# Performance work log

Hardware: AMD Instinct MI355X
Metric: run time of the kernel (lower is better)

The kernel has to match this reference:

```python
import jax, jax.numpy as jnp
import numpy as np

N_NODES = 100000
N_EDGES = 1600000
IN_FEAT = 64
HEADS = 4
OUT_FEAT = 16
NEG_SLOPE = 0.2  # DGL GATConv default


def setup_inputs() -> dict:
    key = jax.random.key(0)
    ks = jax.random.split(key, 6)
    node_feat = jax.random.normal(ks[0], (N_NODES, IN_FEAT), dtype=jnp.float32)
    W = jax.random.normal(ks[1], (IN_FEAT, HEADS * OUT_FEAT), dtype=jnp.float32) * 0.1
    attn_l = jax.random.normal(ks[2], (HEADS, OUT_FEAT), dtype=jnp.float32) * 0.1
    attn_r = jax.random.normal(ks[3], (HEADS, OUT_FEAT), dtype=jnp.float32) * 0.1
    bias = jnp.zeros((HEADS * OUT_FEAT,), dtype=jnp.float32)
    src = jax.random.randint(ks[4], (N_EDGES,), 0, N_NODES, dtype=jnp.int32)
    dst = jax.random.randint(ks[5], (N_EDGES,), 0, N_NODES, dtype=jnp.int32)
    return {"node_feat": node_feat, "W": W, "attn_l": attn_l, "attn_r": attn_r,
            "bias": bias, "src": src, "dst": dst}


def reference(node_feat, W, attn_l, attn_r, bias, src, dst):
    N = node_feat.shape[0]
    H, F = attn_l.shape
    # linear projection: [N, H, F]
    feat = (node_feat @ W).reshape(N, H, F)
    # per-node attention logits: [N, H]
    el = jnp.einsum('nhf,hf->nh', feat, attn_l)
    er = jnp.einsum('nhf,hf->nh', feat, attn_r)
    # per-edge raw score (src contributes el, dst contributes er): [E, H]
    e = jax.nn.leaky_relu(el[src] + er[dst], NEG_SLOPE)
    # segment softmax over incoming edges of each dst node
    emax = jax.ops.segment_max(e, dst, num_segments=N)           # [N, H]
    emax = jnp.where(jnp.isfinite(emax), emax, 0.0)              # zero-in-degree safety
    ex = jnp.exp(e - emax[dst])                                  # [E, H]
    denom = jax.ops.segment_sum(ex, dst, num_segments=N)         # [N, H]
    alpha = ex / denom[dst]                                      # [E, H]
    # weighted scatter-aggregate of projected src features
    msg = feat[src] * alpha[:, :, None]                          # [E, H, F]
    out = jax.ops.segment_sum(msg, dst, num_segments=N)          # [N, H, F]
    out = out + bias.reshape(1, H, F)
    return out.reshape(N, H * F)
```

## Files before the change

kernel.cpp:

```cpp
#include <hip/hip_runtime.h>
#include <math.h>

#define N_NODES 100000
#define N_EDGES 1600000
#define NEG_SLOPE 0.2f
#define NPASS 1

__global__ __launch_bounds__(256) void k1_project(
        const float* __restrict__ x, const float* __restrict__ W,
        const float* __restrict__ attn_l, const float* __restrict__ attn_r,
        float* __restrict__ feat, float* __restrict__ el, float* __restrict__ er,
        int* __restrict__ deg, int* __restrict__ gtotal) {
    int t    = threadIdx.x;
    int lane = t & 63;
    int wib  = t >> 6;
    int h    = lane >> 4;
    if (blockIdx.x == 0 && t == 0) *gtotal = 0;

    float w[64];
    #pragma unroll
    for (int k = 0; k < 64; ++k) w[k] = W[k * 64 + lane];

    float al = attn_l[lane];
    float ar = attn_r[lane];
    int wavesTotal = (gridDim.x * blockDim.x) >> 6;

    for (int n = blockIdx.x * 4 + wib; n < N_NODES; n += wavesTotal) {
        int nu = __builtin_amdgcn_readfirstlane(n);
        const float4* xr = (const float4*)(x + (size_t)nu * 64);
        float a0 = 0.f, a1 = 0.f, a2 = 0.f, a3 = 0.f;
        #pragma unroll
        for (int kq = 0; kq < 16; ++kq) {
            float4 xq = xr[kq];
            a0 = fmaf(xq.x, w[4 * kq + 0], a0);
            a1 = fmaf(xq.y, w[4 * kq + 1], a1);
            a2 = fmaf(xq.z, w[4 * kq + 2], a2);
            a3 = fmaf(xq.w, w[4 * kq + 3], a3);
        }
        float acc = (a0 + a1) + (a2 + a3);
        feat[n * 64 + lane] = acc;
        float vl = acc * al, vr = acc * ar;
        #pragma unroll
        for (int off = 8; off >= 1; off >>= 1) {
            vl += __shfl_xor(vl, off, 64);
            vr += __shfl_xor(vr, off, 64);
        }
        if ((lane & 15) == 0) {
            el[n * 4 + h] = vl;
            er[n * 4 + h] = vr;
        }
        if (lane == 0) deg[n] = 0;
    }
}

__global__ __launch_bounds__(256) void k2_hist_rank(
        const int* __restrict__ dst, int* __restrict__ deg, int* __restrict__ rank) {
    int e = blockIdx.x * blockDim.x + threadIdx.x;
    if (e < N_EDGES) rank[e] = atomicAdd(&deg[dst[e]], 1);
}

__global__ __launch_bounds__(256) void k3_segbase(
        const int* __restrict__ deg, int* __restrict__ rowptr, int* __restrict__ gtotal) {
    int tid  = blockIdx.x * blockDim.x + threadIdx.x;
    int lane = threadIdx.x & 63;
    int n    = tid;
    int dg   = (n < N_NODES) ? deg[n] : 0;
    int incl = dg;
    #pragma unroll
    for (int off = 1; off < 64; off <<= 1) {
        int v = __shfl_up(incl, off, 64);
        if (lane >= off) incl += v;
    }
    int waveTotal = __shfl(incl, 63, 64);
    int base = 0;
    if (lane == 63) base = atomicAdd(gtotal, waveTotal);
    base = __shfl(base, 63, 64);
    if (n < N_NODES) rowptr[n] = base + incl - dg;
}

__global__ __launch_bounds__(256) void k4_fill_phase(
        const int* __restrict__ src, const int* __restrict__ dst,
        const int* __restrict__ rank, const int* __restrict__ rowptr,
        int* __restrict__ edge_src, int lo, int hi) {
    int t = blockIdx.x * blockDim.x + threadIdx.x;
    if (t >= N_EDGES / 4) return;
    int4 d = ((const int4*)dst)[t];
    int4 s = ((const int4*)src)[t];
    int4 r = ((const int4*)rank)[t];
    if (d.x >= lo && d.x < hi) edge_src[rowptr[d.x] + r.x] = s.x;
    if (d.y >= lo && d.y < hi) edge_src[rowptr[d.y] + r.y] = s.y;
    if (d.z >= lo && d.z < hi) edge_src[rowptr[d.z] + r.z] = s.z;
    if (d.w >= lo && d.w < hi) edge_src[rowptr[d.w] + r.w] = s.w;
}

__global__ __launch_bounds__(256) void k5_gather(
        const int* __restrict__ rowptr, const int* __restrict__ deg,
        const int* __restrict__ edge_src,
        const float* __restrict__ el, const float* __restrict__ er,
        const float* __restrict__ feat, const float* __restrict__ bias,
        float* __restrict__ out) {
    int lane = threadIdx.x & 63;
    int h    = lane >> 4;
    int e16  = lane & 15;
    int n    = (blockIdx.x * blockDim.x + threadIdx.x) >> 6;
    if (n >= N_NODES) return;

    int   row0 = rowptr[n];
    int   row1 = row0 + deg[n];
    float er_h = er[n * 4 + h];
    float bv   = bias[lane];
    int   pbase = lane & 48;

    float m = -INFINITY, dnm = 0.f, acc = 0.f;
    for (int base = row0; base < row1; base += 16) {
        int  ei    = base + e16;
        bool valid = ei < row1;
        int  s     = edge_src[valid ? ei : row0];
        float raw  = el[s * 4 + h] + er_h;
        raw = raw > 0.f ? raw : NEG_SLOPE * raw;
        float sc = valid ? raw : -INFINITY;
        float cm = sc;
        cm = fmaxf(cm, __shfl_xor(cm, 1, 64));
        cm = fmaxf(cm, __shfl_xor(cm, 2, 64));
        cm = fmaxf(cm, __shfl_xor(cm, 4, 64));
        cm = fmaxf(cm, __shfl_xor(cm, 8, 64));
        float mn = fmaxf(m, cm);
        float rs = __expf(m - mn);
        float p  = __expf(sc - mn);
        float ps = p;
        ps += __shfl_xor(ps, 1, 64);
        ps += __shfl_xor(ps, 2, 64);
        ps += __shfl_xor(ps, 4, 64);
        ps += __shfl_xor(ps, 8, 64);
        dnm = dnm * rs + ps;
        acc *= rs;
        m = mn;
        #pragma unroll
        for (int j = 0; j < 16; ++j) {
            float pj = __shfl(p, pbase + j, 64);
            int   sj = __shfl(s, j, 64);
            float fa = feat[sj * 64 + lane];
            acc = fmaf(pj, fa, acc);
        }
    }
    out[n * 64 + lane] = (dnm > 0.f ? acc / dnm : 0.f) + bv;
}

extern "C" void kernel_launch(void* const* d_in, const int* in_sizes, int n_in,
                              void* d_out, int out_size, void* d_ws, size_t ws_size,
                              hipStream_t stream) {
    const float* x      = (const float*)d_in[0];
    const float* W      = (const float*)d_in[1];
    const float* attn_l = (const float*)d_in[2];
    const float* attn_r = (const float*)d_in[3];
    const float* bias   = (const float*)d_in[4];
    const int*   src    = (const int*)d_in[5];
    const int*   dst    = (const int*)d_in[6];
    float* out = (float*)d_out;

    float* feat     = (float*)d_ws;
    float* el       = feat + (size_t)N_NODES * 64;
    float* er       = el   + (size_t)N_NODES * 4;
    int*   deg      = (int*)(er + (size_t)N_NODES * 4);
    int*   rowptr   = deg + N_NODES;
    int*   edge_src = rowptr + N_NODES;
    int*   gtotal   = edge_src + N_EDGES;
    int*   rank     = (int*)d_out;

    k1_project<<<2048, 256, 0, stream>>>(x, W, attn_l, attn_r, feat, el, er, deg, gtotal);
    k2_hist_rank<<<(N_EDGES + 255) / 256, 256, 0, stream>>>(dst, deg, rank);
    k3_segbase<<<(N_NODES + 255) / 256, 256, 0, stream>>>(deg, rowptr, gtotal);
    const int nodesPerPass = (N_NODES + NPASS - 1) / NPASS;
    for (int p = 0; p < NPASS; ++p) {
        int lo = p * nodesPerPass;
        int hi = min(N_NODES, lo + nodesPerPass);
        k4_fill_phase<<<(N_EDGES / 4 + 255) / 256, 256, 0, stream>>>(src, dst, rank,
                                                                     rowptr, edge_src, lo, hi);
    }
    k5_gather<<<(N_NODES * 64 + 255) / 256, 256, 0, stream>>>(rowptr, deg, edge_src,
                                                              el, er, feat, bias, out);
}
```

Baseline: 304.2 us.

## Fuse projection and degree histogram into one interleaved kernel

Merges the node projection kernel and the dst-degree histogram/rank kernel into one launch. One block in seven does projection and the rest do atomic histogram work, so the two independent stages run concurrently. Zeroing of deg and gtotal moves to a hipMemsetAsync, which means gtotal is relocated next to deg. This removes one kernel boundary and lets compute-bound and atomic-bound work overlap, at the cost of an extra memset launch and fewer blocks (about 1043) for projection.

```diff
diff --git a/kernel.cpp b/kernel.cpp
--- a/kernel.cpp
+++ b/kernel.cpp
@@ -5,58 +5,58 @@
 #define N_EDGES 1600000
 #define NEG_SLOPE 0.2f
 #define NPASS 1
+#define G_BLOCKS 7296
 
-__global__ __launch_bounds__(256) void k1_project(
+__global__ __launch_bounds__(256) void f1_proj_hist(
         const float* __restrict__ x, const float* __restrict__ W,
         const float* __restrict__ attn_l, const float* __restrict__ attn_r,
+        const int* __restrict__ dst,
         float* __restrict__ feat, float* __restrict__ el, float* __restrict__ er,
-        int* __restrict__ deg, int* __restrict__ gtotal) {
-    int t    = threadIdx.x;
-    int lane = t & 63;
-    int wib  = t >> 6;
-    int h    = lane >> 4;
-    if (blockIdx.x == 0 && t == 0) *gtotal = 0;
-
-    float w[64];
-    #pragma unroll
-    for (int k = 0; k < 64; ++k) w[k] = W[k * 64 + lane];
-
-    float al = attn_l[lane];
-    float ar = attn_r[lane];
-    int wavesTotal = (gridDim.x * blockDim.x) >> 6;
-
-    for (int n = blockIdx.x * 4 + wib; n < N_NODES; n += wavesTotal) {
-        int nu = __builtin_amdgcn_readfirstlane(n);
-        const float4* xr = (const float4*)(x + (size_t)nu * 64);
-        float a0 = 0.f, a1 = 0.f, a2 = 0.f, a3 = 0.f;
+        int* __restrict__ deg, int* __restrict__ rank) {
+    int bid = blockIdx.x;
+    int t   = threadIdx.x;
+    if (bid % 7 == 0) {
+        const int NPROJ = (G_BLOCKS + 6) / 7;
+        int p    = bid / 7;
+        int lane = t & 63;
+        int wib  = t >> 6;
+        int h    = lane >> 4;
+        float w[64];
         #pragma unroll
-        for (int kq = 0; kq < 16; ++kq) {
-            float4 xq = xr[kq];
-            a0 = fmaf(xq.x, w[4 * kq + 0], a0);
-            a1 = fmaf(xq.y, w[4 * kq + 1], a1);
-            a2 = fmaf(xq.z, w[4 * kq + 2], a2);
-            a3 = fmaf(xq.w, w[4 * kq + 3], a3);
+        for (int k = 0; k < 64; ++k) w[k] = W[k * 64 + lane];
+        float al = attn_l[lane];
+        float ar = attn_r[lane];
+        int stride = NPROJ * 4;
+        for (int n = p * 4 + wib; n < N_NODES; n += stride) {
+            int nu = __builtin_amdgcn_readfirstlane(n);
+            const float4* xr = (const float4*)(x + (size_t)nu * 64);
+            float a0 = 0.f, a1 = 0.f, a2 = 0.f, a3 = 0.f;
+            #pragma unroll
+            for (int kq = 0; kq < 16; ++kq) {
+                float4 xq = xr[kq];
+                a0 = fmaf(xq.x, w[4 * kq + 0], a0);
+                a1 = fmaf(xq.y, w[4 * kq + 1], a1);
+                a2 = fmaf(xq.z, w[4 * kq + 2], a2);
+                a3 = fmaf(xq.w, w[4 * kq + 3], a3);
+            }
+            float acc = (a0 + a1) + (a2 + a3);
+            feat[n * 64 + lane] = acc;
+            float vl = acc * al, vr = acc * ar;
+            #pragma unroll
+            for (int off = 8; off >= 1; off >>= 1) {
+                vl += __shfl_xor(vl, off, 64);
+                vr += __shfl_xor(vr, off, 64);
+            }
+            if ((lane & 15) == 0) {
+                el[n * 4 + h] = vl;
+                er[n * 4 + h] = vr;
+            }
         }
-        float acc = (a0 + a1) + (a2 + a3);
-        feat[n * 64 + lane] = acc;
-        float vl = acc * al, vr = acc * ar;
-        #pragma unroll
-        for (int off = 8; off >= 1; off >>= 1) {
-            vl += __shfl_xor(vl, off, 64);
-            vr += __shfl_xor(vr, off, 64);
-        }
-        if ((lane & 15) == 0) {
-            el[n * 4 + h] = vl;
-            er[n * 4 + h] = vr;
-        }
-        if (lane == 0) deg[n] = 0;
+    } else {
+        int hr = bid - (bid + 6) / 7;
+        int e  = hr * 256 + t;
+        if (e < N_EDGES) rank[e] = atomicAdd(&deg[dst[e]], 1);
     }
-}
-
-__global__ __launch_bounds__(256) void k2_hist_rank(
-        const int* __restrict__ dst, int* __restrict__ deg, int* __restrict__ rank) {
-    int e = blockIdx.x * blockDim.x + threadIdx.x;
-    if (e < N_EDGES) rank[e] = atomicAdd(&deg[dst[e]], 1);
 }
 
 __global__ __launch_bounds__(256) void k3_segbase(
@@ -162,13 +162,14 @@
     float* el       = feat + (size_t)N_NODES * 64;
     float* er       = el   + (size_t)N_NODES * 4;
     int*   deg      = (int*)(er + (size_t)N_NODES * 4);
-    int*   rowptr   = deg + N_NODES;
+    int*   gtotal   = deg + N_NODES;
+    int*   rowptr   = gtotal + 1;
     int*   edge_src = rowptr + N_NODES;
-    int*   gtotal   = edge_src + N_EDGES;
     int*   rank     = (int*)d_out;
 
-    k1_project<<<2048, 256, 0, stream>>>(x, W, attn_l, attn_r, feat, el, er, deg, gtotal);
-    k2_hist_rank<<<(N_EDGES + 255) / 256, 256, 0, stream>>>(dst, deg, rank);
+    hipMemsetAsync(deg, 0, (size_t)(N_NODES + 1) * sizeof(int), stream);
+    f1_proj_hist<<<G_BLOCKS, 256, 0, stream>>>(x, W, attn_l, attn_r, dst,
+                                               feat, el, er, deg, rank);
     k3_segbase<<<(N_NODES + 255) / 256, 256, 0, stream>>>(deg, rowptr, gtotal);
     const int nodesPerPass = (N_NODES + NPASS - 1) / NPASS;
     for (int p = 0; p < NPASS; ++p) {
```

New measurement: 290.3 us. -4.6%, faster.
